# Optimization experiments

Hardware: AMD Instinct MI355X
Metric: run time of the kernel (lower is better)

## Reference

```python
import jax, jax.numpy as jnp
import numpy as np
import math

B, S, D, H = 2, 2048, 1024, 16
DH = D // H

def setup_inputs() -> dict:
    key = jax.random.key(0)
    ks = jax.random.split(key, 12)
    s = 1.0 / math.sqrt(D)
    return {
        "q": jax.random.normal(ks[0], (B, S, D), jnp.float32),
        "k": jax.random.normal(ks[1], (B, S, D), jnp.float32),
        "v": jax.random.normal(ks[2], (B, S, D), jnp.float32),
        "mask": jnp.tril(jnp.ones((S, S), dtype=bool)),  # causal mask
        "Wq": jax.random.normal(ks[3], (D, D), jnp.float32) * s,
        "bq": jnp.zeros((D,), jnp.float32),
        "Wk": jax.random.normal(ks[4], (D, D), jnp.float32) * s,
        "bk": jnp.zeros((D,), jnp.float32),
        "Wv": jax.random.normal(ks[5], (D, D), jnp.float32) * s,
        "bv": jnp.zeros((D,), jnp.float32),
        "Wo": jax.random.normal(ks[6], (D, D), jnp.float32) * s,
        "bo": jnp.zeros((D,), jnp.float32),
    }

def _split_heads(x):
    b, s, _ = x.shape
    return x.reshape(b, s, H, DH).transpose(0, 2, 1, 3)  # [B,H,S,DH]

def reference(q, k, v, mask, Wq, bq, Wk, bk, Wv, bv, Wo, bo):
    qh = _split_heads(q @ Wq.T + bq)
    kh = _split_heads(k @ Wk.T + bk)
    vh = _split_heads(v @ Wv.T + bv)
    scale = 1.0 / math.sqrt(DH)
    scores = jnp.einsum('bhqd,bhkd->bhqk', qh, kh) * scale  # [B,H,S,S]
    scores = jnp.where(mask[None, None, :, :], scores, -jnp.inf)
    attn = jax.nn.softmax(scores, axis=-1)
    out = jnp.einsum('bhqk,bhkd->bhqd', attn, vh)  # [B,H,S,DH]
    out = out.transpose(0, 2, 1, 3).reshape(B, S, D)  # combine heads
    return out @ Wo.T + bo
```

## Files before the change

kernel.cpp:

```cpp
#include <hip/hip_runtime.h>

typedef unsigned int u32;
typedef unsigned short u16;
typedef __attribute__((ext_vector_type(8))) short bf16x8;
typedef __attribute__((ext_vector_type(8))) u16 u16x8;
typedef __attribute__((ext_vector_type(4))) u16 u16x4;
typedef __attribute__((ext_vector_type(4))) float f32x4;
typedef __attribute__((ext_vector_type(2))) u32 u32x2;

#define AS1 __attribute__((address_space(1)))
#define AS3 __attribute__((address_space(3)))

__device__ __forceinline__ void gload_lds16(const void* g, void* l) {
  __builtin_amdgcn_global_load_lds((const AS1 u32*)g, (AS3 u32*)l, 16, 0, 0);
}

__device__ __forceinline__ u16 f2bf(float f) {
  union { float f; u32 u; } x; x.f = f;
  u32 u = x.u;
  return (u16)((u + 0x7fffu + ((u >> 16) & 1u)) >> 16);
}

__device__ __forceinline__ u32 cvt_pk_bf16(float lo, float hi) {
  u32 r;
  asm("v_cvt_pk_bf16_f32 %0, %1, %2" : "=v"(r) : "v"(lo), "v"(hi));
  return r;
}

__device__ __forceinline__ float fexp2(float x) {
  float r;
  asm("v_exp_f32 %0, %1" : "=v"(r) : "v"(x));
  return r;
}

__global__ __launch_bounds__(256) void convert_w(
    const float* __restrict__ wq, const float* __restrict__ wk,
    const float* __restrict__ wv, const float* __restrict__ wo,
    u16* __restrict__ dst)
{
  int b = blockIdx.x, t = threadIdx.x;
  int w = b >> 9;
  const float* sp = (w == 0) ? wq : ((w == 1) ? wk : ((w == 2) ? wv : wo));
  size_t lb = (size_t)(b & 511) * 2048 + (size_t)t * 8;
  f32x4 f0 = *(const f32x4*)(sp + lb);
  f32x4 f1 = *(const f32x4*)(sp + lb + 4);
  u16x8 o;
  o[0]=f2bf(f0[0]); o[1]=f2bf(f0[1]); o[2]=f2bf(f0[2]); o[3]=f2bf(f0[3]);
  o[4]=f2bf(f1[0]); o[5]=f2bf(f1[1]); o[6]=f2bf(f1[2]); o[7]=f2bf(f1[3]);
  *(u16x8*)(dst + (size_t)b*2048 + (size_t)t*8) = o;
}

__global__ __launch_bounds__(256, 3) void gemm_qkv(
    const float* __restrict__ Xq, const float* __restrict__ Xk, const float* __restrict__ Xv,
    const u16* __restrict__ Wall,
    const float* __restrict__ bq, const float* __restrict__ bk, const float* __restrict__ bv,
    u16* __restrict__ Cqk, u16* __restrict__ VT)
{
  __shared__ __align__(16) u16 lds[24576];
  const int t = threadIdx.x;
  const int wid = t >> 6, l = t & 63;
  const int c = l & 15, g = l >> 4;
  const int u = blockIdx.x;
  const int lid = (u & 7) * 96 + (u >> 3);
  const int which = lid >> 8;
  const int r5 = lid & 255;
  const int m0 = (r5 >> 3) * 128, n0 = (r5 & 7) * 128;
  const float* Afp = (which == 0) ? Xq : ((which == 1) ? Xk : Xv);
  const u16* Bw = Wall + (size_t)which * 1048576;
  const int wr = wid >> 1, wc = wid & 1;

  const int srow = wid*16 + (l >> 2);
  const int gch = ((l & 3) ^ (srow & 3) ^ ((srow >> 2) & 3)) << 3;
  const float* Ag0 = Afp + (size_t)(m0 + srow)*1024      + gch;
  const float* Ag1 = Afp + (size_t)(m0 + 64 + srow)*1024 + gch;
  const int awr0 = wid*512 + l*8;
  const int awr1 = 2048 + wid*512 + l*8;
  const u16* Bsrc0 = Bw + (size_t)(n0 + srow)*1024      + gch;
  const u16* Bsrc1 = Bw + (size_t)(n0 + 64 + srow)*1024 + gch;
  const int wbase = wid * 512;

  f32x4 ra0, ra1, ra2, ra3;

#define A_LOAD(j) do { \
    const float* ap0_ = Ag0 + ((j) << 5); \
    const float* ap1_ = Ag1 + ((j) << 5); \
    ra0 = *(const f32x4*)ap0_; ra1 = *(const f32x4*)(ap0_ + 4); \
    ra2 = *(const f32x4*)ap1_; ra3 = *(const f32x4*)(ap1_ + 4); \
  } while (0)

#define A_CVT_WRITE(j) do { \
    const int bo_ = ((j) % 3) * 8192; \
    u16x8 w0_, w1_; u32* q0_ = (u32*)&w0_; u32* q1_ = (u32*)&w1_; \
    q0_[0]=cvt_pk_bf16(ra0[0],ra0[1]); q0_[1]=cvt_pk_bf16(ra0[2],ra0[3]); \
    q0_[2]=cvt_pk_bf16(ra1[0],ra1[1]); q0_[3]=cvt_pk_bf16(ra1[2],ra1[3]); \
    q1_[0]=cvt_pk_bf16(ra2[0],ra2[1]); q1_[1]=cvt_pk_bf16(ra2[2],ra2[3]); \
    q1_[2]=cvt_pk_bf16(ra3[0],ra3[1]); q1_[3]=cvt_pk_bf16(ra3[2],ra3[3]); \
    *(u16x8*)&lds[bo_ + awr0] = w0_; \
    *(u16x8*)&lds[bo_ + awr1] = w1_; \
  } while (0)

#define B_STAGE(j) do { \
    const int bo_ = ((j) % 3) * 8192; const int ko_ = (j) << 5; \
    gload_lds16(Bsrc0 + ko_, &lds[bo_ + 4096 + wbase]); \
    gload_lds16(Bsrc1 + ko_, &lds[bo_ + 6144 + wbase]); \
  } while (0)

  const int fswz = (g ^ (c & 3) ^ ((c >> 2) & 3)) << 3;
  const int abase = (wr*64 + c)*32 + fswz;
  const int bbase = 4096 + (wc*64 + c)*32 + fswz;

  f32x4 acc[4][4] = {};

  A_LOAD(0);
  B_STAGE(0);
  B_STAGE(1);
  asm volatile("s_waitcnt vmcnt(2)" ::: "memory");
  A_CVT_WRITE(0);
  A_LOAD(1);
  asm volatile("s_waitcnt lgkmcnt(0)" ::: "memory");
  __builtin_amdgcn_s_barrier();
  __builtin_amdgcn_sched_barrier(0);

#pragma unroll
  for (int tstep = 0; tstep < 32; ++tstep) {
    if (tstep + 2 < 32) B_STAGE(tstep + 2);
    const int bo = (tstep % 3) * 8192;
    bf16x8 af[4], bf[4];
#pragma unroll
    for (int mf = 0; mf < 4; ++mf)
      af[mf] = *(const bf16x8*)&lds[bo + abase + mf*512];
#pragma unroll
    for (int nf = 0; nf < 4; ++nf)
      bf[nf] = *(const bf16x8*)&lds[bo + bbase + nf*512];
    __builtin_amdgcn_s_setprio(1);
#pragma unroll
    for (int mf = 0; mf < 4; ++mf)
#pragma unroll
      for (int nf = 0; nf < 4; ++nf)
        acc[mf][nf] = __builtin_amdgcn_mfma_f32_16x16x32_bf16(af[mf], bf[nf], acc[mf][nf], 0, 0, 0);
    __builtin_amdgcn_s_setprio(0);
    if (tstep + 1 < 32) {
      if (tstep + 2 < 32) asm volatile("s_waitcnt vmcnt(2)" ::: "memory");
      else                asm volatile("s_waitcnt vmcnt(0)" ::: "memory");
      A_CVT_WRITE(tstep + 1);
      if (tstep + 2 < 32) A_LOAD(tstep + 2);
    }
    asm volatile("s_waitcnt lgkmcnt(0)" ::: "memory");
    __builtin_amdgcn_s_barrier();
    __builtin_amdgcn_sched_barrier(0);
  }
#undef A_LOAD
#undef A_CVT_WRITE
#undef B_STAGE

  const float* bias = (which == 0) ? bq : ((which == 1) ? bk : bv);
  if (which < 2) {
#pragma unroll
    for (int mf = 0; mf < 4; ++mf)
#pragma unroll
      for (int nf = 0; nf < 4; ++nf) {
        int row = m0 + wr*64 + mf*16 + g*4;
        int col = n0 + wc*64 + nf*16 + c;
        float bv_ = bias[col];
        int colg = which*1024 + col;
#pragma unroll
        for (int r = 0; r < 4; ++r)
          Cqk[(size_t)(row+r)*2048 + colg] = f2bf(acc[mf][nf][r] + bv_);
      }
  } else {
#pragma unroll
    for (int mf = 0; mf < 4; ++mf)
#pragma unroll
      for (int nf = 0; nf < 4; ++nf) {
        int row = m0 + wr*64 + mf*16 + g*4;
        int col = n0 + wc*64 + nf*16 + c;
        float bv_ = bias[col];
        int bb2 = row >> 11, s = row & 2047;
        int hh = col >> 6, dh = col & 63;
        u16x4 pk;
#pragma unroll
        for (int r = 0; r < 4; ++r) pk[r] = f2bf(acc[mf][nf][r] + bv_);
        *(u16x4*)&VT[((size_t)(((bb2<<4)+hh)<<6) + dh)*2048 + s] = pk;
      }
  }
}

__global__ __launch_bounds__(256, 2) void gemm_out(
    const u16* __restrict__ A, const u16* __restrict__ Bw,
    const float* __restrict__ bias, float* __restrict__ C)
{
  __shared__ __align__(16) u16 lds[18432];
  const int t = threadIdx.x;
  const int wid = t >> 6, l = t & 63;
  const int c = l & 15, g = l >> 4;
  const int u = blockIdx.x;
  const int lid = (u & 7) * 64 + (u >> 3);
  const int m0 = (lid >> 4) * 128, n0 = (lid & 15) * 64;
  const int wr = wid >> 1, wc = wid & 1;

  const int srow = wid*16 + (l >> 2);
  const int sswz = (((l & 3) ^ (srow & 3) ^ ((srow >> 2) & 3)) << 3);
  const u16* Asrc0 = A  + (size_t)(m0 + srow)*1024      + sswz;
  const u16* Asrc1 = A  + (size_t)(m0 + 64 + srow)*1024 + sswz;
  const u16* Bsrc0 = Bw + (size_t)(n0 + srow)*1024      + sswz;
  const int wbase = wid * 512;

#define O_STAGE(j) do { \
    const int bo_ = ((j) % 3) * 6144; const int ko_ = (j) << 5; \
    gload_lds16(Asrc0 + ko_, &lds[bo_ + wbase]); \
    gload_lds16(Asrc1 + ko_, &lds[bo_ + 2048 + wbase]); \
    gload_lds16(Bsrc0 + ko_, &lds[bo_ + 4096 + wbase]); \
  } while (0)

  const int fswz = (g ^ (c & 3) ^ ((c >> 2) & 3)) << 3;
  const int abase = (wr*64 + c)*32 + fswz;
  const int bbase = 4096 + (wc*32 + c)*32 + fswz;

  f32x4 acc[4][2] = {};

  O_STAGE(0);
  O_STAGE(1);
  asm volatile("s_waitcnt vmcnt(3)" ::: "memory");
  __builtin_amdgcn_s_barrier();
  __builtin_amdgcn_sched_barrier(0);

#pragma unroll
  for (int tstep = 0; tstep < 32; ++tstep) {
    if (tstep + 2 < 32) O_STAGE(tstep + 2);
    const int bo = (tstep % 3) * 6144;
    bf16x8 af[4], bf[2];
#pragma unroll
    for (int mf = 0; mf < 4; ++mf)
      af[mf] = *(const bf16x8*)&lds[bo + abase + mf*512];
#pragma unroll
    for (int nf = 0; nf < 2; ++nf)
      bf[nf] = *(const bf16x8*)&lds[bo + bbase + nf*512];
    __builtin_amdgcn_s_setprio(1);
#pragma unroll
    for (int mf = 0; mf < 4; ++mf)
#pragma unroll
      for (int nf = 0; nf < 2; ++nf)
        acc[mf][nf] = __builtin_amdgcn_mfma_f32_16x16x32_bf16(af[mf], bf[nf], acc[mf][nf], 0, 0, 0);
    __builtin_amdgcn_s_setprio(0);
    if (tstep + 2 < 32) asm volatile("s_waitcnt vmcnt(3)" ::: "memory");
    else                asm volatile("s_waitcnt vmcnt(0)" ::: "memory");
    __builtin_amdgcn_s_barrier();
    __builtin_amdgcn_sched_barrier(0);
  }
#undef O_STAGE

#pragma unroll
  for (int mf = 0; mf < 4; ++mf)
#pragma unroll
    for (int nf = 0; nf < 2; ++nf) {
      int row = m0 + wr*64 + mf*16 + g*4;
      int col = n0 + wc*32 + nf*16 + c;
      float bv_ = bias[col];
#pragma unroll
      for (int r = 0; r < 4; ++r)
        C[(size_t)(row+r)*1024 + col] = acc[mf][nf][r] + bv_;
    }
}

__device__ __forceinline__ void stage_kv(u16* lds, const u16* Kt, const u16* Vt,
                                         int buf, int wid) {
#pragma unroll
  for (int ii = 0; ii < 2; ++ii)
    gload_lds16(Kt + (size_t)ii*32*2048, &lds[4096 + buf*4096 + ii*2048 + wid*512]);
#pragma unroll
  for (int ii = 0; ii < 2; ++ii)
    gload_lds16(Vt + (size_t)ii*32*2048, &lds[12288 + buf*4096 + ii*2048 + wid*512]);
}

__device__ __forceinline__ void attn_phase(
    u16* lds, const u16* Qg, const u16* Ka, const u16* Va,
    int q0, int kt0, int nkv, bool maskLast,
    int wid, int g, int c, int arow, int achk, int pbase, int cs,
    float& MI, float& LI, f32x4 (&o)[4])
{
  const float SC = 0.18033688f;
#pragma unroll
  for (int i = 0; i < 2; ++i) {
    int row = i*32 + arow;
    gload_lds16(Qg + (size_t)(q0+row)*2048 + ((achk ^ (row&7)) << 3),
                &lds[i*2048 + wid*512]);
  }
  const u16* Kt = Ka + (size_t)kt0 * (64*2048);
  const u16* Vt = Va + kt0 * 64;
  stage_kv(lds, Kt, Vt, 0, wid);
  asm volatile("s_waitcnt vmcnt(0)" ::: "memory");
  __builtin_amdgcn_s_barrier();
  __builtin_amdgcn_sched_barrier(0);

  bf16x8 qf[2];
#pragma unroll
  for (int kh = 0; kh < 2; ++kh) {
    int row = wid*16 + c;
    int ch = (kh*4 + g) ^ (row & 7);
    qf[kh] = *(const bf16x8*)&lds[row*64 + ch*8];
  }

  float mi = -INFINITY, li = 0.f;
#pragma unroll
  for (int df = 0; df < 4; ++df) o[df] = f32x4{0.f, 0.f, 0.f, 0.f};

  for (int i = 0; i < nkv; ++i) {
    if (i + 1 < nkv) {
      Kt += 64*2048; Vt += 64;
      stage_kv(lds, Kt, Vt, (i+1)&1, wid);
    }
    const u16* Kb = &lds[4096  + (i&1)*4096];
    const u16* Vb = &lds[12288 + (i&1)*4096];

    f32x4 sT[4] = {};
    __builtin_amdgcn_s_setprio(1);
#pragma unroll
    for (int kh = 0; kh < 2; ++kh) {
      bf16x8 kf[4];
#pragma unroll
      for (int nf = 0; nf < 4; ++nf) {
        int row = nf*16 + c;
        int ch = (kh*4 + g) ^ (c & 7);
        kf[nf] = *(const bf16x8*)&Kb[row*64 + ch*8];
      }
#pragma unroll
      for (int nf = 0; nf < 4; ++nf)
        sT[nf] = __builtin_amdgcn_mfma_f32_16x16x32_bf16(kf[nf], qf[kh], sT[nf], 0,0,0);
    }
    __builtin_amdgcn_s_setprio(0);

    if (maskLast && i == nkv - 1) {
#pragma unroll
      for (int nf = 0; nf < 4; ++nf)
#pragma unroll
        for (int r = 0; r < 4; ++r)
          if (nf*16 + g*4 + r > wid*16 + c) sT[nf][r] = -INFINITY;
    }

    float mx = fmaxf(fmaxf(sT[0][0], sT[0][1]), fmaxf(sT[0][2], sT[0][3]));
#pragma unroll
    for (int nf = 1; nf < 4; ++nf)
      mx = fmaxf(mx, fmaxf(fmaxf(sT[nf][0], sT[nf][1]), fmaxf(sT[nf][2], sT[nf][3])));
    if (!__all(mx * SC <= mi + 8.f)) {
      float mxr = fmaxf(mx, __shfl_xor(mx, 16, 64));
      mxr = fmaxf(mxr, __shfl_xor(mxr, 32, 64));
      float mn = fmaxf(mi, mxr * SC);
      float corr = fexp2(mi - mn);
      li *= corr;
#pragma unroll
      for (int df = 0; df < 4; ++df) {
        o[df][0] *= corr; o[df][1] *= corr;
        o[df][2] *= corr; o[df][3] *= corr;
      }
      mi = mn;
    }
    float sum = 0.f;
#pragma unroll
    for (int nf = 0; nf < 4; ++nf)
#pragma unroll
      for (int r = 0; r < 4; ++r) {
        float pv = fexp2(fmaf(sT[nf][r], SC, -mi));
        sT[nf][r] = pv;
        sum += pv;
      }
    li += sum;

#pragma unroll
    for (int nf = 0; nf < 4; ++nf) {
      u32x2 ww;
      ww[0] = cvt_pk_bf16(sT[nf][0], sT[nf][1]);
      ww[1] = cvt_pk_bf16(sT[nf][2], sT[nf][3]);
      int ch = (2*nf + (g >> 1)) ^ cs;
      *(u32x2*)&lds[pbase + c*64 + ch*8 + (g & 1)*4] = ww;
    }
    asm volatile("s_waitcnt lgkmcnt(0)" ::: "memory");
    __builtin_amdgcn_sched_barrier(0);

    __builtin_amdgcn_s_setprio(1);
#pragma unroll
    for (int kh = 0; kh < 2; ++kh) {
      bf16x8 pfr, vf[4];
      {
        int ch = (kh*4 + g) ^ cs;
        pfr = *(const bf16x8*)&lds[pbase + c*64 + ch*8];
      }
#pragma unroll
      for (int df = 0; df < 4; ++df) {
        int d = df*16 + c;
        int ch = (kh*4 + g) ^ (d & 7);
        vf[df] = *(const bf16x8*)&Vb[d*64 + ch*8];
      }
#pragma unroll
      for (int df = 0; df < 4; ++df)
        o[df] = __builtin_amdgcn_mfma_f32_16x16x32_bf16(vf[df], pfr, o[df], 0,0,0);
    }
    __builtin_amdgcn_s_setprio(0);

    asm volatile("s_waitcnt vmcnt(0)" ::: "memory");
    __builtin_amdgcn_s_barrier();
    __builtin_amdgcn_sched_barrier(0);
  }
  MI = mi; LI = li;
}

__device__ __forceinline__ void store_partial(
    float* __restrict__ part, int slot, int s,
    int wid, int g, int c, float mi, float li_tot, const f32x4 (&o)[4])
{
  float* po = part + (size_t)(slot*2 + s) * 4224;
  int q = wid*16 + c;
#pragma unroll
  for (int df = 0; df < 4; ++df)
    *(f32x4*)&po[q*64 + df*16 + g*4] = o[df];
  if (g == 0) { po[4096 + q] = mi; po[4160 + q] = li_tot; }
}

__global__ __launch_bounds__(256, 4) void attn_fwd(
    const u16* __restrict__ QK, const u16* __restrict__ VT,
    u16* __restrict__ AO, float* __restrict__ part)
{
  __shared__ __align__(16) u16 lds[20480];
  const int t = threadIdx.x;
  const int wid = t >> 6, l = t & 63;
  const int g = l >> 4, c = l & 15;
  const int u = blockIdx.x;
  const int lid = (u & 7) * 128 + (u >> 3);
  const int gx = lid & 31, h = (lid >> 5) & 15, b = lid >> 9;
  const int p = gx >> 1, s = gx & 1;
  const u16* Qg  = QK + (size_t)b * 2048 * 2048 + (size_t)h * 64;
  const u16* Kg  = Qg + 1024;
  const u16* VTg = VT + (size_t)(((b << 4) + h) << 6) * 2048;
  const int arow = t >> 3, achk = t & 7;
  const int pbase = wid * 1024;
  const int cs = (c & 7) ^ ((c >> 3) << 2);
  const u16* Ka = Kg  + (size_t)arow*2048 + ((achk ^ (arow & 7)) << 3);
  const u16* Va = VTg + (size_t)arow*2048 + ((achk ^ (arow & 7)) << 3);
  const int slot = ((b*16 + h)*16 + p);

  float mi, li; f32x4 o[4];

  if (s == 0) {
    attn_phase(lds, Qg, Ka, Va, p*64, 0, p+1, true,
               wid, g, c, arow, achk, pbase, cs, mi, li, o);
    {
      float lt = li + __shfl_xor(li, 16, 64);
      lt += __shfl_xor(lt, 32, 64);
      float nr = 1.f / lt;
      int row = p*64 + wid*16 + c;
      size_t rb = ((size_t)b*2048 + row)*1024 + h*64;
#pragma unroll
      for (int df = 0; df < 4; ++df) {
        u16x4 pk;
        pk[0] = f2bf(o[df][0] * nr); pk[1] = f2bf(o[df][1] * nr);
        pk[2] = f2bf(o[df][2] * nr); pk[3] = f2bf(o[df][3] * nr);
        *(u16x4*)&AO[rb + df*16 + g*4] = pk;
      }
    }
    attn_phase(lds, Qg, Ka, Va, (31-p)*64, 0, 16-p, false,
               wid, g, c, arow, achk, pbase, cs, mi, li, o);
    float lt = li + __shfl_xor(li, 16, 64);
    lt += __shfl_xor(lt, 32, 64);
    store_partial(part, slot, 0, wid, g, c, mi, lt, o);
  } else {
    attn_phase(lds, Qg, Ka, Va, (31-p)*64, 16-p, 16, true,
               wid, g, c, arow, achk, pbase, cs, mi, li, o);
    float lt = li + __shfl_xor(li, 16, 64);
    lt += __shfl_xor(lt, 32, 64);
    store_partial(part, slot, 1, wid, g, c, mi, lt, o);
  }
}

__global__ __launch_bounds__(256) void attn_merge(
    const float* __restrict__ part, u16* __restrict__ AO)
{
  int slot = blockIdx.x;
  int p = slot & 15;
  int h = (slot >> 4) & 15;
  int b = slot >> 8;
  const float* p0 = part + (size_t)slot * 8448;
  const float* p1 = p0 + 4224;
  int t = threadIdx.x;
  int r = t >> 2, c0 = (t & 3) * 16;
  float m0 = p0[4096 + r], m1 = p1[4096 + r];
  float l0 = p0[4160 + r], l1 = p1[4160 + r];
  float m = fmaxf(m0, m1);
  float e0 = exp2f(m0 - m), e1 = exp2f(m1 - m);
  float rl = 1.f / (l0*e0 + l1*e1);
  e0 *= rl; e1 *= rl;
  const f32x4* a0 = (const f32x4*)(p0 + r*64 + c0);
  const f32x4* a1 = (const f32x4*)(p1 + r*64 + c0);
  u16x8 w0, w1;
#pragma unroll
  for (int q4 = 0; q4 < 4; ++q4) {
    f32x4 x = a0[q4], y = a1[q4];
#pragma unroll
    for (int j = 0; j < 4; ++j) {
      u16 bf = f2bf(x[j]*e0 + y[j]*e1);
      if (q4 < 2) w0[q4*4+j] = bf; else w1[(q4-2)*4+j] = bf;
    }
  }
  int qrow = (31 - p)*64 + r;
  size_t ab = ((size_t)b*2048 + qrow)*1024 + h*64 + c0;
  *(u16x8*)&AO[ab]     = w0;
  *(u16x8*)&AO[ab + 8] = w1;
}

extern "C" void kernel_launch(void* const* d_in, const int* in_sizes, int n_in,
                              void* d_out, int out_size, void* d_ws, size_t ws_size,
                              hipStream_t stream)
{
  const float* q  = (const float*)d_in[0];
  const float* k  = (const float*)d_in[1];
  const float* v  = (const float*)d_in[2];
  const float* Wq = (const float*)d_in[4];
  const float* bq = (const float*)d_in[5];
  const float* Wk = (const float*)d_in[6];
  const float* bk = (const float*)d_in[7];
  const float* Wv = (const float*)d_in[8];
  const float* bv = (const float*)d_in[9];
  const float* Wo = (const float*)d_in[10];
  const float* bo = (const float*)d_in[11];
  float* out = (float*)d_out;

  u16* ws   = (u16*)d_ws;
  u16* Wqb  = ws + 12582912;
  u16* Wob  = ws + 15728640;
  u16* QKp  = ws + 16777216;
  u16* VTp  = ws + 25165824;
  u16* AO   = ws + 29360128;

  convert_w<<<2048, 256, 0, stream>>>(Wq, Wk, Wv, Wo, Wqb);

  gemm_qkv<<<768, 256, 0, stream>>>(q, k, v, Wqb, bq, bk, bv, QKp, VTp);

  attn_fwd<<<1024, 256, 0, stream>>>(QKp, VTp, AO, (float*)d_ws);

  attn_merge<<<512, 256, 0, stream>>>((const float*)d_ws, AO);

  gemm_out<<<512, 256, 0, stream>>>(AO, Wob, bo, out);
}
```

Baseline: 103.1 us.

## Load V fragments directly from global memory and store attention partials as bf16

The attention kernel no longer stages V tiles through LDS. Each lane reads its V^T MFMA operand fragments straight from global memory, issuing them around the P write to LDS, which shrinks LDS use from 40KB to 24KB per block and drops the V LDS round trip. Split-K partial outputs are now stored as bf16 rather than fp32, roughly halving partial-buffer traffic between attn_fwd and attn_merge. The costs are uncoalesced, unstaged global loads of V that rely on cache hits, and some extra rounding error in the merged partials.

Measured after the change: 138.2 us. 1.34x slower.

```diff
diff --git a/kernel.cpp b/kernel.cpp
--- a/kernel.cpp
+++ b/kernel.cpp
@@ -19,6 +19,10 @@
   union { float f; u32 u; } x; x.f = f;
   u32 u = x.u;
   return (u16)((u + 0x7fffu + ((u >> 16) & 1u)) >> 16);
+}
+
+__device__ __forceinline__ float bf2f(u16 v) {
+  union { u32 u; float f; } x; x.u = (u32)v << 16; return x.f;
 }
 
 __device__ __forceinline__ u32 cvt_pk_bf16(float lo, float hi) {
@@ -262,18 +266,14 @@
     }
 }
 
-__device__ __forceinline__ void stage_kv(u16* lds, const u16* Kt, const u16* Vt,
-                                         int buf, int wid) {
+__device__ __forceinline__ void stage_k(u16* lds, const u16* Kt, int buf, int wid) {
 #pragma unroll
   for (int ii = 0; ii < 2; ++ii)
     gload_lds16(Kt + (size_t)ii*32*2048, &lds[4096 + buf*4096 + ii*2048 + wid*512]);
-#pragma unroll
-  for (int ii = 0; ii < 2; ++ii)
-    gload_lds16(Vt + (size_t)ii*32*2048, &lds[12288 + buf*4096 + ii*2048 + wid*512]);
 }
 
 __device__ __forceinline__ void attn_phase(
-    u16* lds, const u16* Qg, const u16* Ka, const u16* Va,
+    u16* lds, const u16* Qg, const u16* Ka, const u16* Vl,
     int q0, int kt0, int nkv, bool maskLast,
     int wid, int g, int c, int arow, int achk, int pbase, int cs,
     float& MI, float& LI, f32x4 (&o)[4])
@@ -286,8 +286,8 @@
                 &lds[i*2048 + wid*512]);
   }
   const u16* Kt = Ka + (size_t)kt0 * (64*2048);
-  const u16* Vt = Va + kt0 * 64;
-  stage_kv(lds, Kt, Vt, 0, wid);
+  const u16* Vp = Vl + kt0 * 64;
+  stage_k(lds, Kt, 0, wid);
   asm volatile("s_waitcnt vmcnt(0)" ::: "memory");
   __builtin_amdgcn_s_barrier();
   __builtin_amdgcn_sched_barrier(0);
@@ -306,11 +306,10 @@
 
   for (int i = 0; i < nkv; ++i) {
     if (i + 1 < nkv) {
-      Kt += 64*2048; Vt += 64;
-      stage_kv(lds, Kt, Vt, (i+1)&1, wid);
-    }
-    const u16* Kb = &lds[4096  + (i&1)*4096];
-    const u16* Vb = &lds[12288 + (i&1)*4096];
+      Kt += 64*2048;
+      stage_k(lds, Kt, (i+1)&1, wid);
+    }
+    const u16* Kb = &lds[4096 + (i&1)*4096];
 
     f32x4 sT[4] = {};
     __builtin_amdgcn_s_setprio(1);
@@ -365,6 +364,11 @@
       }
     li += sum;
 
+    bf16x8 vfa[4];
+#pragma unroll
+    for (int df = 0; df < 4; ++df)
+      vfa[df] = *(const bf16x8*)(Vp + (size_t)df*32768);
+
 #pragma unroll
     for (int nf = 0; nf < 4; ++nf) {
       u32x2 ww;
@@ -373,53 +377,61 @@
       int ch = (2*nf + (g >> 1)) ^ cs;
       *(u32x2*)&lds[pbase + c*64 + ch*8 + (g & 1)*4] = ww;
     }
+
+    bf16x8 vfb[4];
+#pragma unroll
+    for (int df = 0; df < 4; ++df)
+      vfb[df] = *(const bf16x8*)(Vp + (size_t)df*32768 + 32);
+
     asm volatile("s_waitcnt lgkmcnt(0)" ::: "memory");
     __builtin_amdgcn_sched_barrier(0);
 
     __builtin_amdgcn_s_setprio(1);
-#pragma unroll
-    for (int kh = 0; kh < 2; ++kh) {
-      bf16x8 pfr, vf[4];
-      {
-        int ch = (kh*4 + g) ^ cs;
-        pfr = *(const bf16x8*)&lds[pbase + c*64 + ch*8];
-      }
-#pragma unroll
-      for (int df = 0; df < 4; ++df) {
-        int d = df*16 + c;
-        int ch = (kh*4 + g) ^ (d & 7);
-        vf[df] = *(const bf16x8*)&Vb[d*64 + ch*8];
-      }
+    {
+      bf16x8 pfr;
+      { int ch = g ^ cs; pfr = *(const bf16x8*)&lds[pbase + c*64 + ch*8]; }
 #pragma unroll
       for (int df = 0; df < 4; ++df)
-        o[df] = __builtin_amdgcn_mfma_f32_16x16x32_bf16(vf[df], pfr, o[df], 0,0,0);
+        o[df] = __builtin_amdgcn_mfma_f32_16x16x32_bf16(vfa[df], pfr, o[df], 0,0,0);
+      { int ch = (4 + g) ^ cs; pfr = *(const bf16x8*)&lds[pbase + c*64 + ch*8]; }
+#pragma unroll
+      for (int df = 0; df < 4; ++df)
+        o[df] = __builtin_amdgcn_mfma_f32_16x16x32_bf16(vfb[df], pfr, o[df], 0,0,0);
     }
     __builtin_amdgcn_s_setprio(0);
 
     asm volatile("s_waitcnt vmcnt(0)" ::: "memory");
     __builtin_amdgcn_s_barrier();
     __builtin_amdgcn_sched_barrier(0);
+    Vp += 64;
   }
   MI = mi; LI = li;
 }
 
 __device__ __forceinline__ void store_partial(
-    float* __restrict__ part, int slot, int s,
+    u16* __restrict__ part, int slot, int s,
     int wid, int g, int c, float mi, float li_tot, const f32x4 (&o)[4])
 {
-  float* po = part + (size_t)(slot*2 + s) * 4224;
+  u16* po = part + (size_t)(slot*2 + s) * 4608;
   int q = wid*16 + c;
 #pragma unroll
-  for (int df = 0; df < 4; ++df)
-    *(f32x4*)&po[q*64 + df*16 + g*4] = o[df];
-  if (g == 0) { po[4096 + q] = mi; po[4160 + q] = li_tot; }
+  for (int df = 0; df < 4; ++df) {
+    u16x4 pk;
+    pk[0] = f2bf(o[df][0]); pk[1] = f2bf(o[df][1]);
+    pk[2] = f2bf(o[df][2]); pk[3] = f2bf(o[df][3]);
+    *(u16x4*)&po[q*64 + df*16 + g*4] = pk;
+  }
+  if (g == 0) {
+    ((float*)(po + 4096))[q] = mi;
+    ((float*)(po + 4224))[q] = li_tot;
+  }
 }
 
 __global__ __launch_bounds__(256, 4) void attn_fwd(
     const u16* __restrict__ QK, const u16* __restrict__ VT,
-    u16* __restrict__ AO, float* __restrict__ part)
-{
-  __shared__ __align__(16) u16 lds[20480];
+    u16* __restrict__ AO, u16* __restrict__ part)
+{
+  __shared__ __align__(16) u16 lds[12288];
   const int t = threadIdx.x;
   const int wid = t >> 6, l = t & 63;
   const int g = l >> 4, c = l & 15;
@@ -434,13 +446,13 @@
   const int pbase = wid * 1024;
   const int cs = (c & 7) ^ ((c >> 3) << 2);
   const u16* Ka = Kg  + (size_t)arow*2048 + ((achk ^ (arow & 7)) << 3);
-  const u16* Va = VTg + (size_t)arow*2048 + ((achk ^ (arow & 7)) << 3);
+  const u16* Vl = VTg + (size_t)c*2048 + g*8;
   const int slot = ((b*16 + h)*16 + p);
 
   float mi, li; f32x4 o[4];
 
   if (s == 0) {
-    attn_phase(lds, Qg, Ka, Va, p*64, 0, p+1, true,
+    attn_phase(lds, Qg, Ka, Vl, p*64, 0, p+1, true,
                wid, g, c, arow, achk, pbase, cs, mi, li, o);
     {
       float lt = li + __shfl_xor(li, 16, 64);
@@ -456,13 +468,13 @@
         *(u16x4*)&AO[rb + df*16 + g*4] = pk;
       }
     }
-    attn_phase(lds, Qg, Ka, Va, (31-p)*64, 0, 16-p, false,
+    attn_phase(lds, Qg, Ka, Vl, (31-p)*64, 0, 16-p, false,
                wid, g, c, arow, achk, pbase, cs, mi, li, o);
     float lt = li + __shfl_xor(li, 16, 64);
     lt += __shfl_xor(lt, 32, 64);
     store_partial(part, slot, 0, wid, g, c, mi, lt, o);
   } else {
-    attn_phase(lds, Qg, Ka, Va, (31-p)*64, 16-p, 16, true,
+    attn_phase(lds, Qg, Ka, Vl, (31-p)*64, 16-p, 16, true,
                wid, g, c, arow, achk, pbase, cs, mi, li, o);
     float lt = li + __shfl_xor(li, 16, 64);
     lt += __shfl_xor(lt, 32, 64);
@@ -471,38 +483,35 @@
 }
 
 __global__ __launch_bounds__(256) void attn_merge(
-    const float* __restrict__ part, u16* __restrict__ AO)
+    const u16* __restrict__ part, u16* __restrict__ AO)
 {
   int slot = blockIdx.x;
   int p = slot & 15;
   int h = (slot >> 4) & 15;
   int b = slot >> 8;
-  const float* p0 = part + (size_t)slot * 8448;
-  const float* p1 = p0 + 4224;
+  const u16* p0 = part + (size_t)slot * 9216;
+  const u16* p1 = p0 + 4608;
   int t = threadIdx.x;
   int r = t >> 2, c0 = (t & 3) * 16;
-  float m0 = p0[4096 + r], m1 = p1[4096 + r];
-  float l0 = p0[4160 + r], l1 = p1[4160 + r];
+  float m0 = ((const float*)(p0 + 4096))[r], m1 = ((const float*)(p1 + 4096))[r];
+  float l0 = ((const float*)(p0 + 4224))[r], l1 = ((const float*)(p1 + 4224))[r];
   float m = fmaxf(m0, m1);
   float e0 = exp2f(m0 - m), e1 = exp2f(m1 - m);
   float rl = 1.f / (l0*e0 + l1*e1);
   e0 *= rl; e1 *= rl;
-  const f32x4* a0 = (const f32x4*)(p0 + r*64 + c0);
-  const f32x4* a1 = (const f32x4*)(p1 + r*64 + c0);
-  u16x8 w0, w1;
-#pragma unroll
-  for (int q4 = 0; q4 < 4; ++q4) {
-    f32x4 x = a0[q4], y = a1[q4];
-#pragma unroll
-    for (int j = 0; j < 4; ++j) {
-      u16 bf = f2bf(x[j]*e0 + y[j]*e1);
-      if (q4 < 2) w0[q4*4+j] = bf; else w1[(q4-2)*4+j] = bf;
-    }
-  }
+  const u16x8* a0 = (const u16x8*)(p0 + r*64 + c0);
+  const u16x8* a1 = (const u16x8*)(p1 + r*64 + c0);
   int qrow = (31 - p)*64 + r;
   size_t ab = ((size_t)b*2048 + qrow)*1024 + h*64 + c0;
-  *(u16x8*)&AO[ab]     = w0;
-  *(u16x8*)&AO[ab + 8] = w1;
+#pragma unroll
+  for (int half = 0; half < 2; ++half) {
+    u16x8 x = a0[half], y = a1[half];
+    u16x8 w;
+#pragma unroll
+    for (int j = 0; j < 8; ++j)
+      w[j] = f2bf(bf2f(x[j])*e0 + bf2f(y[j])*e1);
+    *(u16x8*)&AO[ab + half*8] = w;
+  }
 }
 
 extern "C" void kernel_launch(void* const* d_in, const int* in_sizes, int n_in,
@@ -533,9 +542,9 @@
 
   gemm_qkv<<<768, 256, 0, stream>>>(q, k, v, Wqb, bq, bk, bv, QKp, VTp);
 
-  attn_fwd<<<1024, 256, 0, stream>>>(QKp, VTp, AO, (float*)d_ws);
-
-  attn_merge<<<512, 256, 0, stream>>>((const float*)d_ws, AO);
+  attn_fwd<<<1024, 256, 0, stream>>>(QKp, VTp, AO, ws);
+
+  attn_merge<<<512, 256, 0, stream>>>(ws, AO);
 
   gemm_out<<<512, 256, 0, stream>>>(AO, Wob, bo, out);
 }
```
